# Kernel tuning notes

Hardware: AMD Instinct MI355X
Metric: run time of the kernel (lower is better)

## Reference

```python
import jax, jax.numpy as jnp
import numpy as np

BS, H = 2048, 1024
XDIM = 2048 + 4 * 64  # x + R*W = 2304
IN = XDIM + 2 * H     # 4352


def setup_inputs() -> dict:
    key = jax.random.key(0)
    ks = jax.random.split(key, 11)
    s = 1.0 / np.sqrt(IN)  # torch Linear default init scale
    return {
        "input_x": jax.random.normal(ks[0], (BS, XDIM), jnp.float32),
        "previous_time": jax.random.normal(ks[1], (BS, H), jnp.float32),
        "previous_layer": jax.random.normal(ks[2], (BS, H), jnp.float32),
        "old_state": jnp.zeros((BS, H), jnp.float32),
        "Wi": jax.random.normal(ks[3], (H, IN), jnp.float32) * s,
        "bi": jax.random.normal(ks[4], (H,), jnp.float32) * s,
        "Wf": jax.random.normal(ks[5], (H, IN), jnp.float32) * s,
        "bf": jax.random.normal(ks[6], (H,), jnp.float32) * s,
        "Wo": jax.random.normal(ks[7], (H, IN), jnp.float32) * s,
        "bo": jax.random.normal(ks[8], (H,), jnp.float32) * s,
        "Ws": jax.random.normal(ks[9], (H, IN), jnp.float32) * s,
        "bs_state": jax.random.normal(ks[10], (H,), jnp.float32) * s,
    }


def reference(input_x, previous_time, previous_layer, old_state,
              Wi, bi, Wf, bf, Wo, bo, Ws, bs_state):
    # semicolon_input: [bs, x + R*W + 2h]
    z = jnp.concatenate([input_x, previous_time, previous_layer], axis=1)
    # Fuse the four projections into one GEMM: [bs, 4h]
    W_all = jnp.concatenate([Wi, Wf, Wo, Ws], axis=0)          # [4h, IN]
    b_all = jnp.concatenate([bi, bf, bo, bs_state], axis=0)    # [4h]
    proj = z @ W_all.T + b_all
    gi, gf, go, gs = jnp.split(proj, 4, axis=1)
    input_gate = jax.nn.sigmoid(gi)
    forget_gate = jax.nn.sigmoid(gf)
    output_gate = jax.nn.sigmoid(go)
    new_state = forget_gate * old_state + input_gate * jnp.tanh(gs)
    new_hidden = output_gate * jnp.tanh(new_state)
    return new_hidden
```

## Files before the change

kernel.cpp:

```cpp
#include <hip/hip_runtime.h>
#include <stdint.h>
#include <stddef.h>

#define M_DIM 2048
#define N_DIM 4096
#define K_DIM 4352
#define H_DIM 1024
#define X_DIM 2304

#define A_OFF 0u
#define B_OFF 17825792u

typedef __bf16 bf16x8 __attribute__((ext_vector_type(8)));
typedef float f32x4 __attribute__((ext_vector_type(4)));

__device__ __forceinline__ unsigned short f32_to_bf16(float f) {
    unsigned u = __float_as_uint(f);
    u += 0x7FFFu + ((u >> 16) & 1u);
    return (unsigned short)(u >> 16);
}

__device__ __forceinline__ float sigm_(float x) { return 1.f / (1.f + __expf(-x)); }
__device__ __forceinline__ float tanh_(float x) {
    x = fminf(15.f, fmaxf(-15.f, x));
    float e = __expf(2.f * x);
    return (e - 1.f) / (e + 1.f);
}

__global__ __launch_bounds__(256) void convert_kernel(
    const float* __restrict__ x, const float* __restrict__ pt,
    const float* __restrict__ pl,
    const float* __restrict__ Wi, const float* __restrict__ Wf,
    const float* __restrict__ Wo, const float* __restrict__ Ws,
    unsigned short* __restrict__ Abf, unsigned short* __restrict__ Bbf)
{
    const int row = blockIdx.x;
    const float* srow = nullptr;
    unsigned short* drow;
    if (row < M_DIM) {
        drow = Abf + (size_t)row * K_DIM;
    } else {
        int n = row - M_DIM;
        int g = n >> 10, h = n & 1023;
        const float* W = (g == 0) ? Wi : (g == 1) ? Wf : (g == 2) ? Wo : Ws;
        srow = W + (size_t)h * K_DIM;
        drow = Bbf + (size_t)(h * 4 + g) * K_DIM;
    }

    for (int c8 = threadIdx.x; c8 < K_DIM / 8; c8 += 256) {
        int col = c8 * 8;
        const float* s;
        if (row < M_DIM) {
            if (col < X_DIM)              s = x  + (size_t)row * X_DIM + col;
            else if (col < X_DIM + H_DIM) s = pt + (size_t)row * H_DIM + (col - X_DIM);
            else                          s = pl + (size_t)row * H_DIM + (col - X_DIM - H_DIM);
        } else {
            s = srow + col;
        }
        float4 v0 = ((const float4*)s)[0];
        float4 v1 = ((const float4*)s)[1];
        union { unsigned short h[8]; uint4 u; } r;
        r.h[0] = f32_to_bf16(v0.x); r.h[1] = f32_to_bf16(v0.y);
        r.h[2] = f32_to_bf16(v0.z); r.h[3] = f32_to_bf16(v0.w);
        r.h[4] = f32_to_bf16(v1.x); r.h[5] = f32_to_bf16(v1.y);
        r.h[6] = f32_to_bf16(v1.z); r.h[7] = f32_to_bf16(v1.w);
        *(uint4*)(drow + col) = r.u;
    }
}

__global__ __launch_bounds__(512, 2) void gemm_fused(
    const unsigned short* __restrict__ A,
    const unsigned short* __restrict__ B,
    const float* __restrict__ old_state,
    const float* __restrict__ bi, const float* __restrict__ bfv,
    const float* __restrict__ bo, const float* __restrict__ bs,
    float* __restrict__ out)
{
    __shared__ __align__(16) char smem[98304];
    float* sP = (float*)smem;

    const int tid  = threadIdx.x;
    const int lane = tid & 63;
    const int wave = tid >> 6;
    const int wm = (wave >> 2) * 64;
    const int wn = (wave & 3) * 64;

    const int b   = blockIdx.x;
    const int xcd = b & 7;
    const int j   = b >> 3;
    const int m0  = (j >> 1) * 128;
    const int n0  = (xcd * 2 + (j & 1)) * 256;

    const int srow_ = tid >> 2;
    const int kb_   = (tid & 3) ^ ((tid >> 3) & 3);
    const unsigned short* Asrc  = A + (size_t)(m0 + srow_)       * K_DIM + kb_ * 8;
    const unsigned short* Bsrc0 = B + (size_t)(n0 + srow_)       * K_DIM + kb_ * 8;
    const unsigned short* Bsrc1 = B + (size_t)(n0 + 128 + srow_) * K_DIM + kb_ * 8;

    const int fr  = lane & 15;
    const int kb0 = lane >> 4;
    const int swz = (kb0 ^ ((fr >> 1) & 3)) * 16;
    const int aoff = (wm + fr) * 64 + swz;
    const int boff = 8192 + (wn + fr) * 64 + swz;

    f32x4 acc[4][4];
#pragma unroll
    for (int i = 0; i < 4; ++i)
#pragma unroll
        for (int jj = 0; jj < 4; ++jj) acc[i][jj] = (f32x4){0.f, 0.f, 0.f, 0.f};

    auto stage = [&](int h, int c) {
        const size_t koff = (size_t)h * 32;
        __builtin_amdgcn_global_load_lds(
            (const __attribute__((address_space(1))) unsigned*)(Asrc + koff),
            (__attribute__((address_space(3))) unsigned*)(smem + c * 24576 + wave * 1024),
            16, 0, 0);
        __builtin_amdgcn_global_load_lds(
            (const __attribute__((address_space(1))) unsigned*)(Bsrc0 + koff),
            (__attribute__((address_space(3))) unsigned*)(smem + c * 24576 + 8192 + wave * 1024),
            16, 0, 0);
        __builtin_amdgcn_global_load_lds(
            (const __attribute__((address_space(1))) unsigned*)(Bsrc1 + koff),
            (__attribute__((address_space(3))) unsigned*)(smem + c * 24576 + 16384 + wave * 1024),
            16, 0, 0);
    };

#define VM6 asm volatile("s_waitcnt vmcnt(6)" ::: "memory")
#define VM3 asm volatile("s_waitcnt vmcnt(3)" ::: "memory")
#define VM0 asm volatile("s_waitcnt vmcnt(0)" ::: "memory")
#define VMNONE ((void)0)

#define PHASE(C, SH, DOSTAGE, VMLINE)                                           \
    do {                                                                        \
        bf16x8 af[4], bq[4];                                                    \
        _Pragma("unroll")                                                       \
        for (int i_ = 0; i_ < 4; ++i_) {                                        \
            af[i_] = *(const bf16x8*)(smem + (C) * 24576 + aoff + i_ * 1024);   \
            bq[i_] = *(const bf16x8*)(smem + (C) * 24576 + boff + i_ * 1024);   \
        }                                                                       \
        if (DOSTAGE) stage((SH), ((C) + 3) & 3);                                \
        __builtin_amdgcn_s_barrier();                                           \
        asm volatile("s_waitcnt lgkmcnt(0)" ::: "memory");                      \
        __builtin_amdgcn_sched_barrier(0);                                      \
        __builtin_amdgcn_s_setprio(1);                                          \
        _Pragma("unroll")                                                       \
        for (int i_ = 0; i_ < 4; ++i_)                                          \
            _Pragma("unroll")                                                   \
            for (int j_ = 0; j_ < 4; ++j_)                                      \
                acc[i_][j_] = __builtin_amdgcn_mfma_f32_16x16x32_bf16(          \
                    af[i_], bq[j_], acc[i_][j_], 0, 0, 0);                      \
        __builtin_amdgcn_s_setprio(0);                                          \
        __builtin_amdgcn_sched_barrier(0);                                      \
        VMLINE;                                                                 \
        __builtin_amdgcn_s_barrier();                                           \
    } while (0)

    stage(0, 0); stage(1, 1); stage(2, 2);
    VM6;
    __builtin_amdgcn_s_barrier();

    for (int h4 = 0; h4 < 132; h4 += 4) {
        PHASE(0, h4 + 3, true, VM6);
        PHASE(1, h4 + 4, true, VM6);
        PHASE(2, h4 + 5, true, VM6);
        PHASE(3, h4 + 6, true, VM6);
    }
    PHASE(0, 135, true,  VM6);
    PHASE(1, 0,   false, VM3);
    PHASE(2, 0,   false, VM0);
    PHASE(3, 0,   false, VMNONE);

#undef PHASE
#undef VM6
#undef VM3
#undef VM0
#undef VMNONE

    const int cw = lane & 15;
    const int rw = (lane >> 4) * 4;
    const int hl = tid & 15;
    const int rb = tid >> 4;

    for (int p = 0; p < 4; ++p) {
        __syncthreads();
        if ((wave & 3) == p) {
#pragma unroll
            for (int i = 0; i < 4; ++i)
#pragma unroll
                for (int jj = 0; jj < 4; ++jj)
#pragma unroll
                    for (int r = 0; r < 4; ++r)
                        sP[(wm + i * 16 + rw + r) * 76 + jj * 16 + cw] = acc[i][jj][r];
        }
        __syncthreads();

        const int hg = (n0 >> 2) + p * 16 + hl;
        const float b_i = bi[hg], b_f = bfv[hg], b_o = bo[hg], b_s = bs[hg];
#pragma unroll
        for (int k = 0; k < 4; ++k) {
            const int row = rb + 32 * k;
            float4 g = *(const float4*)(sP + row * 76 + hl * 4);
            const size_t oidx = (size_t)(m0 + row) * H_DIM + hg;
            float old = old_state[oidx];
            float ig = sigm_(g.x + b_i);
            float fg = sigm_(g.y + b_f);
            float og = sigm_(g.z + b_o);
            float ts = tanh_(g.w + b_s);
            out[oidx] = og * tanh_(fg * old + ig * ts);
        }
    }
}

extern "C" void kernel_launch(void* const* d_in, const int* in_sizes, int n_in,
                              void* d_out, int out_size, void* d_ws, size_t ws_size,
                              hipStream_t stream) {
    const float* x   = (const float*)d_in[0];
    const float* pt  = (const float*)d_in[1];
    const float* pl  = (const float*)d_in[2];
    const float* old = (const float*)d_in[3];
    const float* Wi  = (const float*)d_in[4];
    const float* bi  = (const float*)d_in[5];
    const float* Wf  = (const float*)d_in[6];
    const float* bf  = (const float*)d_in[7];
    const float* Wo  = (const float*)d_in[8];
    const float* bo  = (const float*)d_in[9];
    const float* Ws  = (const float*)d_in[10];
    const float* bs  = (const float*)d_in[11];
    float* out = (float*)d_out;

    char* ws = (char*)d_ws;
    unsigned short* Abf = (unsigned short*)(ws + A_OFF);
    unsigned short* Bbf = (unsigned short*)(ws + B_OFF);

    convert_kernel<<<M_DIM + N_DIM, 256, 0, stream>>>(x, pt, pl, Wi, Wf, Wo, Ws, Abf, Bbf);

    gemm_fused<<<256, 512, 0, stream>>>(Abf, Bbf, old, bi, bf, bo, bs, out);
}
```

Measured before the change: 231.7 us.

## Restructure GEMM mainloop to 64-wide K tiles with triple-buffered quarter-phase pipeline

```diff
diff --git a/kernel.cpp b/kernel.cpp
--- a/kernel.cpp
+++ b/kernel.cpp
@@ -76,7 +76,7 @@
     const float* __restrict__ bo, const float* __restrict__ bs,
     float* __restrict__ out)
 {
-    __shared__ __align__(16) char smem[98304];
+    __shared__ __align__(16) char smem[147456];
     float* sP = (float*)smem;
 
     const int tid  = threadIdx.x;
@@ -91,17 +91,18 @@
     const int m0  = (j >> 1) * 128;
     const int n0  = (xcd * 2 + (j & 1)) * 256;
 
-    const int srow_ = tid >> 2;
-    const int kb_   = (tid & 3) ^ ((tid >> 3) & 3);
-    const unsigned short* Asrc  = A + (size_t)(m0 + srow_)       * K_DIM + kb_ * 8;
-    const unsigned short* Bsrc0 = B + (size_t)(n0 + srow_)       * K_DIM + kb_ * 8;
-    const unsigned short* Bsrc1 = B + (size_t)(n0 + 128 + srow_) * K_DIM + kb_ * 8;
+    const int urow = tid >> 3;
+    const int ukb  = (tid & 7) ^ ((tid >> 3) & 7);
+    const unsigned short* Asrc = A + (size_t)(m0 + urow) * K_DIM + ukb * 8;
+    const unsigned short* Bsrc = B + (size_t)(n0 + urow) * K_DIM + ukb * 8;
 
     const int fr  = lane & 15;
     const int kb0 = lane >> 4;
-    const int swz = (kb0 ^ ((fr >> 1) & 3)) * 16;
-    const int aoff = (wm + fr) * 64 + swz;
-    const int boff = 8192 + (wn + fr) * 64 + swz;
+    const int sw  = fr & 7;
+    const int sK0 = ((kb0    ) ^ sw) * 16;
+    const int sK1 = ((kb0 ^ 4) ^ sw) * 16;
+    const int aRow =         (wm + fr) * 128;
+    const int bRow = 16384 + (wn + fr) * 128;
 
     f32x4 acc[4][4];
 #pragma unroll
@@ -109,72 +110,140 @@
 #pragma unroll
         for (int jj = 0; jj < 4; ++jj) acc[i][jj] = (f32x4){0.f, 0.f, 0.f, 0.f};
 
-    auto stage = [&](int h, int c) {
-        const size_t koff = (size_t)h * 32;
-        __builtin_amdgcn_global_load_lds(
-            (const __attribute__((address_space(1))) unsigned*)(Asrc + koff),
-            (__attribute__((address_space(3))) unsigned*)(smem + c * 24576 + wave * 1024),
-            16, 0, 0);
-        __builtin_amdgcn_global_load_lds(
-            (const __attribute__((address_space(1))) unsigned*)(Bsrc0 + koff),
-            (__attribute__((address_space(3))) unsigned*)(smem + c * 24576 + 8192 + wave * 1024),
-            16, 0, 0);
-        __builtin_amdgcn_global_load_lds(
-            (const __attribute__((address_space(1))) unsigned*)(Bsrc1 + koff),
-            (__attribute__((address_space(3))) unsigned*)(smem + c * 24576 + 16384 + wave * 1024),
-            16, 0, 0);
+    bf16x8 aF[4], bF[4], bG[4];
+
+#define GLDS(GP, LP) __builtin_amdgcn_global_load_lds(                          \
+        (const __attribute__((address_space(1))) unsigned*)(GP),                \
+        (__attribute__((address_space(3))) unsigned*)(LP), 16, 0, 0)
+
+    auto STAGE3a = [&](int t, int cs) {
+        const size_t ko = (size_t)t * 64;
+        char* base = smem + cs * 49152;
+        GLDS(Asrc + ko,                     base +             wave * 1024);
+        GLDS(Asrc + (size_t)64  * K_DIM + ko, base + 8192    + wave * 1024);
+        GLDS(Bsrc + ko,                     base + 16384     + wave * 1024);
     };
+    auto STAGE3b = [&](int t, int cs) {
+        const size_t ko = (size_t)t * 64;
+        char* base = smem + cs * 49152 + 16384;
+        GLDS(Bsrc + (size_t)64  * K_DIM + ko, base + 8192  + wave * 1024);
+        GLDS(Bsrc + (size_t)128 * K_DIM + ko, base + 16384 + wave * 1024);
+        GLDS(Bsrc + (size_t)192 * K_DIM + ko, base + 24576 + wave * 1024);
+    };
+
+#define RD_Q0(C) {                                                              \
+        const char* bb_ = smem + (C) * 49152;                                   \
+        aF[0] = *(const bf16x8*)(bb_ + aRow + 0 * 2048 + sK0);                  \
+        aF[1] = *(const bf16x8*)(bb_ + aRow + 1 * 2048 + sK0);                  \
+        bF[0] = *(const bf16x8*)(bb_ + bRow + 0 * 2048 + sK0);                  \
+        bF[1] = *(const bf16x8*)(bb_ + bRow + 1 * 2048 + sK0); }
+#define RD_Q1(C) {                                                              \
+        const char* bb_ = smem + (C) * 49152;                                   \
+        aF[2] = *(const bf16x8*)(bb_ + aRow + 2 * 2048 + sK0);                  \
+        aF[3] = *(const bf16x8*)(bb_ + aRow + 3 * 2048 + sK0);                  \
+        bF[2] = *(const bf16x8*)(bb_ + bRow + 2 * 2048 + sK0);                  \
+        bF[3] = *(const bf16x8*)(bb_ + bRow + 3 * 2048 + sK0); }
+#define RD_Q2(C) {                                                              \
+        const char* bb_ = smem + (C) * 49152;                                   \
+        aF[0] = *(const bf16x8*)(bb_ + aRow + 0 * 2048 + sK1);                  \
+        aF[1] = *(const bf16x8*)(bb_ + aRow + 1 * 2048 + sK1);                  \
+        bG[0] = *(const bf16x8*)(bb_ + bRow + 0 * 2048 + sK1);                  \
+        bG[1] = *(const bf16x8*)(bb_ + bRow + 1 * 2048 + sK1); }
+#define RD_Q3(C) {                                                              \
+        const char* bb_ = smem + (C) * 49152;                                   \
+        aF[2] = *(const bf16x8*)(bb_ + aRow + 2 * 2048 + sK1);                  \
+        aF[3] = *(const bf16x8*)(bb_ + aRow + 3 * 2048 + sK1);                  \
+        bG[2] = *(const bf16x8*)(bb_ + bRow + 2 * 2048 + sK1);                  \
+        bG[3] = *(const bf16x8*)(bb_ + bRow + 3 * 2048 + sK1); }
+
+#define MM(I0, I1, BB)                                                          \
+    _Pragma("unroll")                                                           \
+    for (int j_ = 0; j_ < 4; ++j_) {                                            \
+        acc[I0][j_] = __builtin_amdgcn_mfma_f32_16x16x32_bf16(                  \
+            aF[(I0) & 1 ? 1 : 0 + ((I0) >= 2 ? 2 : 0)], BB[j_], acc[I0][j_], 0, 0, 0); \
+        acc[I1][j_] = __builtin_amdgcn_mfma_f32_16x16x32_bf16(                  \
+            aF[(I1) & 1 ? ((I1) >= 2 ? 3 : 1) : 2], BB[j_], acc[I1][j_], 0, 0, 0); \
+    }
+#undef MM
+#define MM_Q0                                                                   \
+    _Pragma("unroll")                                                           \
+    for (int j_ = 0; j_ < 4; ++j_) {                                            \
+        acc[0][j_] = __builtin_amdgcn_mfma_f32_16x16x32_bf16(aF[0], bF[j_], acc[0][j_], 0, 0, 0); \
+        acc[1][j_] = __builtin_amdgcn_mfma_f32_16x16x32_bf16(aF[1], bF[j_], acc[1][j_], 0, 0, 0); }
+#define MM_Q1                                                                   \
+    _Pragma("unroll")                                                           \
+    for (int j_ = 0; j_ < 4; ++j_) {                                            \
+        acc[2][j_] = __builtin_amdgcn_mfma_f32_16x16x32_bf16(aF[2], bF[j_], acc[2][j_], 0, 0, 0); \
+        acc[3][j_] = __builtin_amdgcn_mfma_f32_16x16x32_bf16(aF[3], bF[j_], acc[3][j_], 0, 0, 0); }
+#define MM_Q2                                                                   \
+    _Pragma("unroll")                                                           \
+    for (int j_ = 0; j_ < 4; ++j_) {                                            \
+        acc[0][j_] = __builtin_amdgcn_mfma_f32_16x16x32_bf16(aF[0], bG[j_], acc[0][j_], 0, 0, 0); \
+        acc[1][j_] = __builtin_amdgcn_mfma_f32_16x16x32_bf16(aF[1], bG[j_], acc[1][j_], 0, 0, 0); }
+#define MM_Q3                                                                   \
+    _Pragma("unroll")                                                           \
+    for (int j_ = 0; j_ < 4; ++j_) {                                            \
+        acc[2][j_] = __builtin_amdgcn_mfma_f32_16x16x32_bf16(aF[2], bG[j_], acc[2][j_], 0, 0, 0); \
+        acc[3][j_] = __builtin_amdgcn_mfma_f32_16x16x32_bf16(aF[3], bG[j_], acc[3][j_], 0, 0, 0); }
 
 #define VM6 asm volatile("s_waitcnt vmcnt(6)" ::: "memory")
-#define VM3 asm volatile("s_waitcnt vmcnt(3)" ::: "memory")
 #define VM0 asm volatile("s_waitcnt vmcnt(0)" ::: "memory")
-#define VMNONE ((void)0)
-
-#define PHASE(C, SH, DOSTAGE, VMLINE)                                           \
+
+#define PH(RDLINE, STLINE, MMLINE, VMLINE)                                      \
     do {                                                                        \
-        bf16x8 af[4], bq[4];                                                    \
-        _Pragma("unroll")                                                       \
-        for (int i_ = 0; i_ < 4; ++i_) {                                        \
-            af[i_] = *(const bf16x8*)(smem + (C) * 24576 + aoff + i_ * 1024);   \
-            bq[i_] = *(const bf16x8*)(smem + (C) * 24576 + boff + i_ * 1024);   \
-        }                                                                       \
-        if (DOSTAGE) stage((SH), ((C) + 3) & 3);                                \
+        RDLINE; STLINE;                                                         \
+        __builtin_amdgcn_sched_barrier(0);                                      \
         __builtin_amdgcn_s_barrier();                                           \
-        asm volatile("s_waitcnt lgkmcnt(0)" ::: "memory");                      \
-        __builtin_amdgcn_sched_barrier(0);                                      \
         __builtin_amdgcn_s_setprio(1);                                          \
-        _Pragma("unroll")                                                       \
-        for (int i_ = 0; i_ < 4; ++i_)                                          \
-            _Pragma("unroll")                                                   \
-            for (int j_ = 0; j_ < 4; ++j_)                                      \
-                acc[i_][j_] = __builtin_amdgcn_mfma_f32_16x16x32_bf16(          \
-                    af[i_], bq[j_], acc[i_][j_], 0, 0, 0);                      \
+        MMLINE;                                                                 \
         __builtin_amdgcn_s_setprio(0);                                          \
         __builtin_amdgcn_sched_barrier(0);                                      \
         VMLINE;                                                                 \
         __builtin_amdgcn_s_barrier();                                           \
     } while (0)
 
-    stage(0, 0); stage(1, 1); stage(2, 2);
+#define TILE(C, CN, CS, T)                                                      \
+    PH(RD_Q1(C), STAGE3a((T) + 2, CS), MM_Q0, (void)0);                         \
+    PH(RD_Q2(C), STAGE3b((T) + 2, CS), MM_Q1, (void)0);                         \
+    PH(RD_Q3(C), (void)0,              MM_Q2, VM6);                             \
+    PH(RD_Q0(CN), (void)0,             MM_Q3, (void)0);
+
+    STAGE3a(0, 0); STAGE3b(0, 0);
+    STAGE3a(1, 1); STAGE3b(1, 1);
     VM6;
     __builtin_amdgcn_s_barrier();
-
-    for (int h4 = 0; h4 < 132; h4 += 4) {
-        PHASE(0, h4 + 3, true, VM6);
-        PHASE(1, h4 + 4, true, VM6);
-        PHASE(2, h4 + 5, true, VM6);
-        PHASE(3, h4 + 6, true, VM6);
-    }
-    PHASE(0, 135, true,  VM6);
-    PHASE(1, 0,   false, VM3);
-    PHASE(2, 0,   false, VM0);
-    PHASE(3, 0,   false, VMNONE);
-
-#undef PHASE
+    RD_Q0(0);
+
+    for (int it = 0; it < 22; ++it) {
+        const int t = it * 3;
+        TILE(0, 1, 2, t);
+        TILE(1, 2, 0, t + 1);
+        TILE(2, 0, 1, t + 2);
+    }
+    PH(RD_Q1(0), (void)0, MM_Q0, (void)0);
+    PH(RD_Q2(0), (void)0, MM_Q1, (void)0);
+    PH(RD_Q3(0), (void)0, MM_Q2, VM0);
+    PH(RD_Q0(1), (void)0, MM_Q3, (void)0);
+    PH(RD_Q1(1), (void)0, MM_Q0, (void)0);
+    PH(RD_Q2(1), (void)0, MM_Q1, (void)0);
+    PH(RD_Q3(1), (void)0, MM_Q2, (void)0);
+    __builtin_amdgcn_s_setprio(1);
+    MM_Q3;
+    __builtin_amdgcn_s_setprio(0);
+
+#undef TILE
+#undef PH
 #undef VM6
-#undef VM3
 #undef VM0
-#undef VMNONE
+#undef MM_Q0
+#undef MM_Q1
+#undef MM_Q2
+#undef MM_Q3
+#undef RD_Q0
+#undef RD_Q1
+#undef RD_Q2
+#undef RD_Q3
+#undef GLDS
 
     const int cw = lane & 15;
     const int rw = (lane >> 4) * 4;
```

Result: faster. 225.9 us (-2.5%).
